# Performance work log

Measured on AMD Instinct MI355X. Metric: run time of the kernel, lower is better.

Reference implementation:

```python
import jax, jax.numpy as jnp
import numpy as np
import math

KMAX = 4
K_FLOOR = 1e-6
NUM_GRAPHS = 32

def _k_lattice():
    r = np.arange(-KMAX, KMAX + 1)
    I, J, Kk = np.meshgrid(r, r, r, indexing='ij')
    lat = np.stack([I, J, Kk], axis=-1).reshape(-1, 3).astype(np.float32)
    lat = lat[np.any(lat != 0, axis=1)]  # exclude k=0 (include_k0=False)
    return jnp.asarray(lat)  # [K,3], K=728

def setup_inputs() -> dict:
    key = jax.random.key(0)
    ks = jax.random.split(key, 10)
    N, B, C, H = 8192, NUM_GRAPHS, 4, 64
    pos = jax.random.uniform(ks[0], (N, 3), dtype=jnp.float32) * 10.0
    batch = jnp.sort(jax.random.randint(ks[1], (N,), 0, B)).astype(jnp.int32)
    cell = jnp.eye(3, dtype=jnp.float32)[None] * 12.0 + 0.2 * jax.random.normal(ks[2], (B, 3, 3), dtype=jnp.float32)
    source = 0.1 * jax.random.normal(ks[3], (N, C), dtype=jnp.float32)
    W1 = jax.random.normal(ks[4], (3, H), dtype=jnp.float32) * (1.0 / math.sqrt(3))
    b1 = jnp.zeros((H,), jnp.float32)
    W2 = jax.random.normal(ks[5], (H, H), dtype=jnp.float32) * (1.0 / math.sqrt(H))
    b2 = jnp.zeros((H,), jnp.float32)
    W3 = jax.random.normal(ks[6], (H, 1), dtype=jnp.float32) * (1.0 / math.sqrt(H))
    b3 = jnp.zeros((1,), jnp.float32)
    return {"pos": pos, "batch": batch, "cell": cell, "source": source,
            "W1": W1, "b1": b1, "W2": W2, "b2": b2, "W3": W3, "b3": b3}

def reference(pos, batch, cell, source, W1, b1, W2, b2, W3, b3):
    two_pi = 2.0 * math.pi
    klat = _k_lattice()                              # [K,3]
    B = cell.shape[0]
    inv_cells = jnp.linalg.inv(cell)                 # [B,3,3]
    # fractional coords and phases
    frac = jnp.einsum('ni,nij->nj', pos, inv_cells[batch])   # [N,3]
    phases = two_pi * (frac @ klat.T)                # [N,K]
    cosP = jnp.cos(phases)
    sinP = jnp.sin(phases)
    # structure factors via segment-sum over graphs
    w_cos = source[:, None, :] * cosP[:, :, None]    # [N,K,C]
    w_sin = source[:, None, :] * sinP[:, :, None]
    S_cos = jax.ops.segment_sum(w_cos, batch, num_segments=B)  # [B,K,C]
    S_sin = jax.ops.segment_sum(w_sin, batch, num_segments=B)
    # k-space radial filter
    k_cart = two_pi * jnp.einsum('kd,bdh->bkh', klat, inv_cells)  # [B,K,3]
    k_norms = jnp.linalg.norm(k_cart, axis=-1)       # [B,K]
    safe_k = jnp.maximum(k_norms, K_FLOOR)
    x0 = jnp.log1p(safe_k)
    feat = jnp.stack([x0, x0 * x0, 1.0 / safe_k], axis=-1)       # [B,K,3]
    h = jax.nn.silu(feat @ W1 + b1)
    h = jax.nn.silu(h @ W2 + b2)
    scale = jax.nn.softplus((h @ W3 + b3)[..., 0])   # [B,K]
    w = (4.0 * math.pi / (safe_k * safe_k)) * scale
    w = jnp.where(k_norms > K_FLOOR, w, 0.0)         # include_k0=False
    volumes = jnp.maximum(jnp.abs(jnp.linalg.det(cell)), K_FLOOR)  # [B]
    # per-atom potential
    t_cos = w[batch] * cosP                          # [N,K]
    t_sin = w[batch] * sinP
    potential = (jnp.einsum('nk,nkc->nc', t_cos, S_cos[batch]) +
                 jnp.einsum('nk,nkc->nc', t_sin, S_sin[batch])) / volumes[batch][:, None]
    atom_energy = 0.5 * jnp.sum(source * potential, axis=-1, keepdims=True)  # [N,1]
    return atom_energy
```

## Files before the change

kernel.cpp:

```cpp
#include <hip/hip_runtime.h>
#include <math.h>

#define N_ATOMS 8192
#define NGRAPH  32
#define KHALF   364
#define TWO_PI  6.28318530717958647692f


__device__ __forceinline__ float silu_f(float x) {
    return x / (1.0f + __expf(-x));
}

__device__ __forceinline__ void screv(float rev, float* s, float* c) {
    float f = rev - floorf(rev);
    *s = __builtin_amdgcn_sinf(f);
    *c = __builtin_amdgcn_cosf(f);
}

__device__ __forceinline__ void inv3x3(const float* __restrict__ c, float* iv, float* detOut) {
    float a00 = c[0], a01 = c[1], a02 = c[2];
    float a10 = c[3], a11 = c[4], a12 = c[5];
    float a20 = c[6], a21 = c[7], a22 = c[8];
    float c00 = a11 * a22 - a12 * a21;
    float c01 = a12 * a20 - a10 * a22;
    float c02 = a10 * a21 - a11 * a20;
    float det = a00 * c00 + a01 * c01 + a02 * c02;
    float r = 1.0f / det;
    iv[0] = c00 * r; iv[1] = (a02 * a21 - a01 * a22) * r; iv[2] = (a01 * a12 - a02 * a11) * r;
    iv[3] = c01 * r; iv[4] = (a00 * a22 - a02 * a20) * r; iv[5] = (a02 * a10 - a00 * a12) * r;
    iv[6] = c02 * r; iv[7] = (a01 * a20 - a00 * a21) * r; iv[8] = (a00 * a11 - a01 * a10) * r;
    *detOut = det;
}

__device__ __forceinline__ int lower_bound_wave(const int* __restrict__ batch, int v, int lane) {
    int x = batch[lane * 128];
    int c1 = __popcll(__ballot(x < v));
    int lo2 = (c1 > 0 ? c1 - 1 : 0) * 128;
    int y = batch[lo2 + lane * 2];
    int c2 = __popcll(__ballot(y < v));
    if (c2 == 0) return lo2;
    int cand = lo2 + 2 * c2;
    return (batch[cand - 1] < v) ? cand : cand - 1;
}

__device__ __forceinline__ void tab_fill(float2* __restrict__ t9, float c1, float s1) {
    float c2 = c1 * c1 - s1 * s1, s2 = 2.f * c1 * s1;
    float c3 = c2 * c1 - s2 * s1, s3 = c2 * s1 + s2 * c1;
    float c4 = c2 * c2 - s2 * s2, s4 = 2.f * c2 * s2;
    t9[4] = make_float2(1.f, 0.f);
    t9[5] = make_float2(c1, s1);
    t9[3] = make_float2(c1, -s1);
    t9[6] = make_float2(c2, s2);
    t9[2] = make_float2(c2, -s2);
    t9[7] = make_float2(c3, s3);
    t9[1] = make_float2(c3, -s3);
    t9[8] = make_float2(c4, s4);
    t9[0] = make_float2(c4, -s4);
}

__global__ __launch_bounds__(256) void kAll(
    const float* __restrict__ cell, const float* __restrict__ pos,
    const int* __restrict__ batch, const float* __restrict__ source,
    const float* __restrict__ W1, const float* __restrict__ b1,
    const float* __restrict__ W2, const float* __restrict__ b2,
    const float* __restrict__ W3, const float* __restrict__ b3,
    float* __restrict__ out)
{
    __shared__ float2 tab[128][3][9];
    __shared__ float4 srcs[128];
    __shared__ float4 partC[3][64];
    __shared__ float4 partS[3][64];
    __shared__ float  comb[256];
    __shared__ int    sbounds[2];
    __shared__ float  lw[45];
    __shared__ float4 lSc[64];
    __shared__ float4 lSs[64];

    int bid = blockIdx.x;
    int tid = threadIdx.x;
    int gb    = bid / 9;
    int slice = bid - gb * 9;
    int p  = (slice < 8) ? (slice >> 1) : 4;
    int ah = (slice < 8) ? (slice & 1) : 0;
    int j0   = ah ? 5 : 0;
    int j1   = ah ? 9 : 5;
    int nel  = ah ? 36 : 45;
    int eoff = j0 * 9;

    int kl = tid & 63;
    int h  = tid >> 6;

    if (h >= 2) {
        int lb = lower_bound_wave(batch, gb + (h - 2), kl);
        if (kl == 0) sbounds[h - 2] = lb;
    }

    float iv[9]; float det;
    inv3x3(cell + gb * 9, iv, &det);
    float vol = fmaxf(fabsf(det), 1e-6f);

    {
        int el = kl;
        int hk = p * 81 + eoff + el;
        bool evalid = (el < nel) && (hk < KHALF);
        int ek = evalid ? hk : 0;
        float fi = (float)(ek / 81 - 4);
        float fj = (float)((ek / 9) % 9 - 4);
        float fl = (float)(ek % 9 - 4);
        float kx = TWO_PI * (fi * iv[0] + fj * iv[3] + fl * iv[6]);
        float ky = TWO_PI * (fi * iv[1] + fj * iv[4] + fl * iv[7]);
        float kz = TWO_PI * (fi * iv[2] + fj * iv[5] + fl * iv[8]);
        float kn = sqrtf(kx * kx + ky * ky + kz * kz);
        float sk = fmaxf(kn, 1e-6f);
        float x0 = log1pf(sk);
        float f0 = x0, f1 = x0 * x0, f2 = 1.0f / sk;

        float acc[16];
        #pragma unroll
        for (int j = 0; j < 16; ++j) acc[j] = b2[h * 16 + j];
        for (int i = 0; i < 64; ++i) {
            float a = b1[i] + f0 * W1[i] + f1 * W1[64 + i] + f2 * W1[128 + i];
            float hh = silu_f(a);
            const float* w2row = W2 + i * 64 + h * 16;
            #pragma unroll
            for (int j = 0; j < 16; ++j) acc[j] = fmaf(hh, w2row[j], acc[j]);
        }
        float partial = 0.f;
        #pragma unroll
        for (int j = 0; j < 16; ++j) partial += silu_f(acc[j]) * W3[h * 16 + j];
        comb[tid] = partial;
        __syncthreads();
        if (h == 0) {
            float mlp = b3[0] + comb[kl] + comb[64 + kl] + comb[128 + kl] + comb[192 + kl];
            float sc = (mlp > 20.0f) ? mlp : log1pf(__expf(mlp));
            float wgt = (12.566370614359172954f / (sk * sk)) * sc;
            if (!(kn > 1e-6f)) wgt = 0.0f;
            if (kl < nel) lw[kl] = evalid ? (wgt / vol) : 0.0f;
        }
    }

    int s0 = sbounds[0], e0 = sbounds[1];

    bool kvalid = (kl < nel) && (p * 81 + eoff + kl < KHALF);
    int eg  = eoff + (kvalid ? kl : 0);
    int jp4 = eg / 9;
    int lp4 = eg - jp4 * 9;

    float4 accC = make_float4(0.f, 0.f, 0.f, 0.f);
    float4 accS = make_float4(0.f, 0.f, 0.f, 0.f);

    for (int base = s0; base < e0; base += 128) {
        int cnt = min(128, e0 - base);
        __syncthreads();
        {
            int a    = tid & 127;
            int dsel = tid >> 7;
            if (a < cnt) {
                int n = base + a;
                float px = pos[n * 3], py = pos[n * 3 + 1], pz = pos[n * 3 + 2];
                int d = dsel;
                float ph = px * iv[d] + py * iv[3 + d] + pz * iv[6 + d];
                float s1, c1; screv(ph, &s1, &c1);
                tab_fill(&tab[a][d][0], c1, s1);
                if (dsel == 0) {
                    float ph2 = px * iv[2] + py * iv[5] + pz * iv[8];
                    float s2_, c2_; screv(ph2, &s2_, &c2_);
                    tab_fill(&tab[a][2][0], c2_, s2_);
                } else {
                    srcs[a] = ((const float4*)source)[n];
                }
            }
        }
        __syncthreads();

        if (kvalid) {
            for (int a = h; a < cnt; a += 4) {
                float2 ti = tab[a][0][p];
                float2 tj = tab[a][1][jp4];
                float2 tl = tab[a][2][lp4];
                float c12 = ti.x * tj.x - ti.y * tj.y;
                float s12 = ti.x * tj.y + ti.y * tj.x;
                float cv = c12 * tl.x - s12 * tl.y;
                float sv = c12 * tl.y + s12 * tl.x;
                float4 s = srcs[a];
                accC.x = fmaf(s.x, cv, accC.x); accC.y = fmaf(s.y, cv, accC.y);
                accC.z = fmaf(s.z, cv, accC.z); accC.w = fmaf(s.w, cv, accC.w);
                accS.x = fmaf(s.x, sv, accS.x); accS.y = fmaf(s.y, sv, accS.y);
                accS.z = fmaf(s.z, sv, accS.z); accS.w = fmaf(s.w, sv, accS.w);
            }
        }
    }

    if (h > 0) {
        partC[h - 1][kl] = accC;
        partS[h - 1][kl] = accS;
    }
    __syncthreads();
    if (h == 0) {
        #pragma unroll
        for (int qq = 0; qq < 3; ++qq) {
            float4 pc = partC[qq][kl], ps = partS[qq][kl];
            accC.x += pc.x; accC.y += pc.y; accC.z += pc.z; accC.w += pc.w;
            accS.x += ps.x; accS.y += ps.y; accS.z += ps.z; accS.w += ps.w;
        }
        lSc[kl] = accC;
        lSs[kl] = accS;
    }
    __syncthreads();

    int g = 4 - p;

    for (int n = s0 + tid; n < e0; n += 256) {
        float px = pos[n * 3], py = pos[n * 3 + 1], pz = pos[n * 3 + 2];
        float p1 = px * iv[0] + py * iv[3] + pz * iv[6];
        float p2 = px * iv[1] + py * iv[4] + pz * iv[7];
        float p3 = px * iv[2] + py * iv[5] + pz * iv[8];
        float s1, c1; screv(p1, &s1, &c1);
        float s2, c2; screv(p2, &s2, &c2);
        float s3, c3; screv(p3, &s3, &c3);
        float c3_2 = c3 * c3 - s3 * s3, s3_2 = 2.f * c3 * s3;
        float c3_4 = c3_2 * c3_2 - s3_2 * s3_2, s3_4 = 2.f * c3_2 * s3_2;
        float4 s = ((const float4*)source)[n];

        float cg_, sg_;
        if (g == 0)      { cg_ = 1.f; sg_ = 0.f; }
        else if (g == 1) { cg_ = c1; sg_ = s1; }
        else {
            float c2p = c1 * c1 - s1 * s1, s2p = 2.f * c1 * s1;
            if (g == 2)      { cg_ = c2p; sg_ = s2p; }
            else if (g == 3) { cg_ = c2p * c1 - s2p * s1; sg_ = s2p * c1 + c2p * s1; }
            else             { cg_ = c2p * c2p - s2p * s2p; sg_ = 2.f * c2p * s2p; }
        }
        float ci0 = cg_, si0 = -sg_;

        float ejc, ejs;
        if (ah == 0) {
            float c2_2 = c2 * c2 - s2 * s2, s2_2 = 2.f * c2 * s2;
            float c2_4 = c2_2 * c2_2 - s2_2 * s2_2, s2_4 = 2.f * c2_2 * s2_2;
            ejc = ci0 * c2_4 + si0 * s2_4;
            ejs = si0 * c2_4 - ci0 * s2_4;
        } else {
            ejc = ci0 * c2 - si0 * s2;
            ejs = si0 * c2 + ci0 * s2;
        }

        float acc = 0.f;
        for (int jj = j0; jj < j1; ++jj) {
            float fc = ejc * c3_4 + ejs * s3_4;
            float fs = ejs * c3_4 - ejc * s3_4;
            #pragma unroll
            for (int ll = 0; ll < 9; ++ll) {
                int el = (jj - j0) * 9 + ll;
                float4 C  = lSc[el];
                float4 S4 = lSs[el];
                float w_ = lw[el];
                float dc = s.x * C.x  + s.y * C.y  + s.z * C.z  + s.w * C.w;
                float ds = s.x * S4.x + s.y * S4.y + s.z * S4.z + s.w * S4.w;
                acc = fmaf(w_, fmaf(fc, dc, fs * ds), acc);
                float nfc = fc * c3 - fs * s3;
                fs = fc * s3 + fs * c3;
                fc = nfc;
            }
            float nejc = ejc * c2 - ejs * s2;
            ejs = ejc * s2 + ejs * c2;
            ejc = nejc;
        }
        atomicAdd(&out[n], acc);
    }
}

extern "C" void kernel_launch(void* const* d_in, const int* in_sizes, int n_in,
                              void* d_out, int out_size, void* d_ws, size_t ws_size,
                              hipStream_t stream)
{
    const float* pos    = (const float*)d_in[0];
    const int*   batch  = (const int*)d_in[1];
    const float* cell   = (const float*)d_in[2];
    const float* source = (const float*)d_in[3];
    const float* W1 = (const float*)d_in[4];
    const float* b1 = (const float*)d_in[5];
    const float* W2 = (const float*)d_in[6];
    const float* b2 = (const float*)d_in[7];
    const float* W3 = (const float*)d_in[8];
    const float* b3 = (const float*)d_in[9];
    float* out = (float*)d_out;
    (void)d_ws; (void)ws_size;

    kAll<<<dim3(NGRAPH * 9), 256, 0, stream>>>(cell, pos, batch, source,
        W1, b1, W2, b2, W3, b3, out);
}
```

Measured before the change: 105.9 us.

## Rebalance k-vector partition into 8 blocks per graph, folding the p=4 slice

The k-space half-lattice was split into 9 blocks per graph, with a lightly loaded ninth block for the p=4 plane (41 valid k). The plane is now spread across the four ah=1 blocks, each taking 1 or 2 extra j-rows, so every block handles up to 54-63 k values and the grid shrinks from 288 to 256 blocks. That matches the device's compute-unit count better and removes a wave of under-used work. The cost is an extra per-atom loop segment with its own phase recurrence, plus more k per block in the atom loop.

```diff
diff --git a/kernel.cpp b/kernel.cpp
--- a/kernel.cpp
+++ b/kernel.cpp
@@ -72,20 +72,20 @@
     __shared__ float4 partS[3][64];
     __shared__ float  comb[256];
     __shared__ int    sbounds[2];
-    __shared__ float  lw[45];
+    __shared__ float  lw[64];
     __shared__ float4 lSc[64];
     __shared__ float4 lSs[64];
 
     int bid = blockIdx.x;
     int tid = threadIdx.x;
-    int gb    = bid / 9;
-    int slice = bid - gb * 9;
-    int p  = (slice < 8) ? (slice >> 1) : 4;
-    int ah = (slice < 8) ? (slice & 1) : 0;
-    int j0   = ah ? 5 : 0;
-    int j1   = ah ? 9 : 5;
-    int nel  = ah ? 36 : 45;
-    int eoff = j0 * 9;
+    int gb = bid >> 3;
+    int b  = bid & 7;
+
+    int pA, jA0, jA1, jB0, jB1, nsegA, nel;
+    if (b < 4) { pA = b;     jA0 = 0; jA1 = 5; jB0 = 0; jB1 = 0; nsegA = 45; nel = 45; }
+    else       { pA = b - 4; jA0 = 5; jA1 = 9;
+                 jB0 = b - 4; jB1 = (b == 7) ? 5 : (b - 3);
+                 nsegA = 36; nel = 36 + (jB1 - jB0) * 9; }
 
     int kl = tid & 63;
     int h  = tid >> 6;
@@ -99,14 +99,17 @@
     inv3x3(cell + gb * 9, iv, &det);
     float vol = fmaxf(fabsf(det), 1e-6f);
 
+    int el = kl;
+    int pe, jje, lle;
+    if (el < nsegA) { pe = pA; jje = jA0 + el / 9; lle = el % 9; }
+    else            { int e2 = el - nsegA; pe = 4; jje = jB0 + e2 / 9; lle = e2 % 9; }
+    int hk = pe * 81 + jje * 9 + lle;
+    bool evalid = (el < nel) && (hk < KHALF);
+
     {
-        int el = kl;
-        int hk = p * 81 + eoff + el;
-        bool evalid = (el < nel) && (hk < KHALF);
-        int ek = evalid ? hk : 0;
-        float fi = (float)(ek / 81 - 4);
-        float fj = (float)((ek / 9) % 9 - 4);
-        float fl = (float)(ek % 9 - 4);
+        float fi = (float)(pe - 4);
+        float fj = (float)(jje - 4);
+        float fl = (float)(lle - 4);
         float kx = TWO_PI * (fi * iv[0] + fj * iv[3] + fl * iv[6]);
         float ky = TWO_PI * (fi * iv[1] + fj * iv[4] + fl * iv[7]);
         float kz = TWO_PI * (fi * iv[2] + fj * iv[5] + fl * iv[8]);
@@ -135,16 +138,11 @@
             float sc = (mlp > 20.0f) ? mlp : log1pf(__expf(mlp));
             float wgt = (12.566370614359172954f / (sk * sk)) * sc;
             if (!(kn > 1e-6f)) wgt = 0.0f;
-            if (kl < nel) lw[kl] = evalid ? (wgt / vol) : 0.0f;
+            lw[kl] = evalid ? (wgt / vol) : 0.0f;
         }
     }
 
     int s0 = sbounds[0], e0 = sbounds[1];
-
-    bool kvalid = (kl < nel) && (p * 81 + eoff + kl < KHALF);
-    int eg  = eoff + (kvalid ? kl : 0);
-    int jp4 = eg / 9;
-    int lp4 = eg - jp4 * 9;
 
     float4 accC = make_float4(0.f, 0.f, 0.f, 0.f);
     float4 accS = make_float4(0.f, 0.f, 0.f, 0.f);
@@ -173,11 +171,11 @@
         }
         __syncthreads();
 
-        if (kvalid) {
+        if (evalid) {
             for (int a = h; a < cnt; a += 4) {
-                float2 ti = tab[a][0][p];
-                float2 tj = tab[a][1][jp4];
-                float2 tl = tab[a][2][lp4];
+                float2 ti = tab[a][0][pe];
+                float2 tj = tab[a][1][jje];
+                float2 tl = tab[a][2][lle];
                 float c12 = ti.x * tj.x - ti.y * tj.y;
                 float s12 = ti.x * tj.y + ti.y * tj.x;
                 float cv = c12 * tl.x - s12 * tl.y;
@@ -208,7 +206,7 @@
     }
     __syncthreads();
 
-    int g = 4 - p;
+    int g = 4 - pA;
 
     for (int n = s0 + tid; n < e0; n += 256) {
         float px = pos[n * 3], py = pos[n * 3 + 1], pz = pos[n * 3 + 2];
@@ -220,51 +218,83 @@
         float s3, c3; screv(p3, &s3, &c3);
         float c3_2 = c3 * c3 - s3 * s3, s3_2 = 2.f * c3 * s3;
         float c3_4 = c3_2 * c3_2 - s3_2 * s3_2, s3_4 = 2.f * c3_2 * s3_2;
+        float c2_2 = c2 * c2 - s2 * s2, s2_2 = 2.f * c2 * s2;
+        float c2_4 = c2_2 * c2_2 - s2_2 * s2_2, s2_4 = 2.f * c2_2 * s2_2;
         float4 s = ((const float4*)source)[n];
 
-        float cg_, sg_;
-        if (g == 0)      { cg_ = 1.f; sg_ = 0.f; }
-        else if (g == 1) { cg_ = c1; sg_ = s1; }
-        else {
-            float c2p = c1 * c1 - s1 * s1, s2p = 2.f * c1 * s1;
-            if (g == 2)      { cg_ = c2p; sg_ = s2p; }
-            else if (g == 3) { cg_ = c2p * c1 - s2p * s1; sg_ = s2p * c1 + c2p * s1; }
-            else             { cg_ = c2p * c2p - s2p * s2p; sg_ = 2.f * c2p * s2p; }
-        }
-        float ci0 = cg_, si0 = -sg_;
-
-        float ejc, ejs;
-        if (ah == 0) {
-            float c2_2 = c2 * c2 - s2 * s2, s2_2 = 2.f * c2 * s2;
-            float c2_4 = c2_2 * c2_2 - s2_2 * s2_2, s2_4 = 2.f * c2_2 * s2_2;
-            ejc = ci0 * c2_4 + si0 * s2_4;
-            ejs = si0 * c2_4 - ci0 * s2_4;
-        } else {
-            ejc = ci0 * c2 - si0 * s2;
-            ejs = si0 * c2 + ci0 * s2;
-        }
-
         float acc = 0.f;
-        for (int jj = j0; jj < j1; ++jj) {
-            float fc = ejc * c3_4 + ejs * s3_4;
-            float fs = ejs * c3_4 - ejc * s3_4;
-            #pragma unroll
-            for (int ll = 0; ll < 9; ++ll) {
-                int el = (jj - j0) * 9 + ll;
-                float4 C  = lSc[el];
-                float4 S4 = lSs[el];
-                float w_ = lw[el];
-                float dc = s.x * C.x  + s.y * C.y  + s.z * C.z  + s.w * C.w;
-                float ds = s.x * S4.x + s.y * S4.y + s.z * S4.z + s.w * S4.w;
-                acc = fmaf(w_, fmaf(fc, dc, fs * ds), acc);
-                float nfc = fc * c3 - fs * s3;
-                fs = fc * s3 + fs * c3;
-                fc = nfc;
-            }
-            float nejc = ejc * c2 - ejs * s2;
-            ejs = ejc * s2 + ejs * c2;
-            ejc = nejc;
-        }
+
+        {
+            float cg_, sg_;
+            if (g == 1)      { cg_ = c1; sg_ = s1; }
+            else {
+                float c2p = c1 * c1 - s1 * s1, s2p = 2.f * c1 * s1;
+                if (g == 2)      { cg_ = c2p; sg_ = s2p; }
+                else if (g == 3) { cg_ = c2p * c1 - s2p * s1; sg_ = s2p * c1 + c2p * s1; }
+                else             { cg_ = c2p * c2p - s2p * s2p; sg_ = 2.f * c2p * s2p; }
+            }
+            float ci0 = cg_, si0 = -sg_;
+
+            float ejc, ejs;
+            if (jA0 == 0) {
+                ejc = ci0 * c2_4 + si0 * s2_4;
+                ejs = si0 * c2_4 - ci0 * s2_4;
+            } else {
+                ejc = ci0 * c2 - si0 * s2;
+                ejs = si0 * c2 + ci0 * s2;
+            }
+
+            for (int jj = jA0; jj < jA1; ++jj) {
+                float fc = ejc * c3_4 + ejs * s3_4;
+                float fs = ejs * c3_4 - ejc * s3_4;
+                #pragma unroll
+                for (int ll = 0; ll < 9; ++ll) {
+                    int e = (jj - jA0) * 9 + ll;
+                    float4 C  = lSc[e];
+                    float4 S4 = lSs[e];
+                    float w_ = lw[e];
+                    float dc = s.x * C.x  + s.y * C.y  + s.z * C.z  + s.w * C.w;
+                    float ds = s.x * S4.x + s.y * S4.y + s.z * S4.z + s.w * S4.w;
+                    acc = fmaf(w_, fmaf(fc, dc, fs * ds), acc);
+                    float nfc = fc * c3 - fs * s3;
+                    fs = fc * s3 + fs * c3;
+                    fc = nfc;
+                }
+                float nejc = ejc * c2 - ejs * s2;
+                ejs = ejc * s2 + ejs * c2;
+                ejc = nejc;
+            }
+        }
+
+        if (jB1 > jB0) {
+            float ejc = c2_4, ejs = -s2_4;
+            for (int t = 0; t < jB0; ++t) {
+                float nf = ejc * c2 - ejs * s2;
+                ejs = ejc * s2 + ejs * c2;
+                ejc = nf;
+            }
+            for (int jj = jB0; jj < jB1; ++jj) {
+                float fc = ejc * c3_4 + ejs * s3_4;
+                float fs = ejs * c3_4 - ejc * s3_4;
+                #pragma unroll
+                for (int ll = 0; ll < 9; ++ll) {
+                    int e = nsegA + (jj - jB0) * 9 + ll;
+                    float4 C  = lSc[e];
+                    float4 S4 = lSs[e];
+                    float w_ = lw[e];
+                    float dc = s.x * C.x  + s.y * C.y  + s.z * C.z  + s.w * C.w;
+                    float ds = s.x * S4.x + s.y * S4.y + s.z * S4.z + s.w * S4.w;
+                    acc = fmaf(w_, fmaf(fc, dc, fs * ds), acc);
+                    float nfc = fc * c3 - fs * s3;
+                    fs = fc * s3 + fs * c3;
+                    fc = nfc;
+                }
+                float nejc = ejc * c2 - ejs * s2;
+                ejs = ejc * s2 + ejs * c2;
+                ejc = nejc;
+            }
+        }
+
         atomicAdd(&out[n], acc);
     }
 }
@@ -286,6 +316,6 @@
     float* out = (float*)d_out;
     (void)d_ws; (void)ws_size;
 
-    kAll<<<dim3(NGRAPH * 9), 256, 0, stream>>>(cell, pos, batch, source,
+    kAll<<<dim3(NGRAPH * 8), 256, 0, stream>>>(cell, pos, batch, source,
         W1, b1, W2, b2, W3, b3, out);
 }
```

Result: faster. 99.15 us (-6.3%).
